# Performance work log

Measured on AMD Instinct MI355X. Metric: run time of the kernel, lower is better.

The kernel has to match this reference:

```python
import jax, jax.numpy as jnp
import numpy as np

SIGMA = (2.0, 5.0, 10.0, 20.0, 40.0, 60.0)  # RBF bandwidths from __init__
MAX_SEG = 16  # static upper bound on number of class segments (== n classes in gt)


def setup_inputs() -> dict:
    key = jax.random.key(0)
    k1, k2, k3 = jax.random.split(key, 3)
    B, C, H, W = 1, 128, 64, 64
    predict = jax.random.normal(k1, (B, C, H, W), dtype=jnp.float32)
    target = jax.random.normal(k2, (B, C, H, W), dtype=jnp.float32)
    # sorted_randint -> contiguous variable-size class segments, as the torch loop assumes
    gt = jnp.sort(jax.random.randint(k3, (B * H * W,), 0, MAX_SEG)).reshape(B, H, W)
    ignore_mask = jnp.ones((B, H, W), dtype=bool)  # all pixels visible
    return {"predict": predict, "target": target, "gt": gt, "ignore_mask": ignore_mask}


def _sqdist(a, b):
    # ||a_i - b_j||^2 ; prob_mat in the original is -0.5 * this
    aa = jnp.sum(a * a, axis=1)
    bb = jnp.sum(b * b, axis=1)
    return aa[:, None] + bb[None, :] - 2.0 * (a @ b.T)


def reference(predict, target, gt, ignore_mask):
    d = predict.shape[1]
    # [B,C,H,W] -> [V,C]; ignore_mask is all True so visible set == all pixels
    pf = predict.transpose(0, 2, 3, 1).reshape(-1, d)
    tf = target.transpose(0, 2, 3, 1).reshape(-1, d)
    cls = gt.reshape(-1)

    # segment id = index of contiguous class run (what the Python boundary loop computes)
    boundary = (cls[1:] != cls[:-1]).astype(jnp.int32)
    seg = jnp.concatenate([jnp.zeros((1,), jnp.int32), jnp.cumsum(boundary)])
    counts = jax.ops.segment_sum(jnp.ones(seg.shape, predict.dtype), seg, num_segments=MAX_SEG)

    # pairwise squared distances within/between predict and target (shared across segments)
    Dpp = _sqdist(pf, pf)
    Dtt = _sqdist(tf, tf)
    Dpt = _sqdist(pf, tf)

    # Per segment with M=N=n: ww is +1/(2n^2) on pp/tt blocks, -1/(2n^2) on cross blocks,
    # and sum over the tp block equals sum over the pt block. So
    # loss_s = (1/(2 n^2)) * sum_bw sum_{i,j in s} (Kpp + Ktt - 2 Kpt)_{ij}
    C = jnp.zeros_like(Dpp)
    for bw in SIGMA:
        inv = -0.5 / bw  # K = exp(prob/bw) = exp(-||x_i-x_j||^2 / (2 bw))
        C = C + jnp.exp(inv * Dpp) + jnp.exp(inv * Dtt) - 2.0 * jnp.exp(inv * Dpt)

    same = seg[:, None] == seg[None, :]
    C = jnp.where(same, C, 0.0)
    seg_tot = jax.ops.segment_sum(jnp.sum(C, axis=1), seg, num_segments=MAX_SEG)

    denom = jnp.maximum(2.0 * counts * counts, 1.0)
    loss_s = jnp.where(counts > 0, seg_tot / denom, 0.0)
    pos = loss_s > 0
    loss_s = jnp.where(pos, jnp.sqrt(jnp.where(pos, loss_s, 1.0)), 0.0)  # sqrt(loss) if >0 else 0

    class_count = jnp.sum(counts > 0).astype(predict.dtype)
    return jnp.sum(loss_s) / class_count
```

## Files before the change

### kernel.cpp

```cpp
#include <hip/hip_runtime.h>
#include <math.h>

#define NCLS 16
#define TILE 32
#define PAD  36
#define NB   2048
#define PIXB 16

typedef float vfloat4 __attribute__((ext_vector_type(4), aligned(4)));

struct Ctl {
    int   counts[NCLS];
    int   starts[NCLS + 1];
    int   tpc[NCLS];
    int   pairBase[NCLS + 1];
    float classSum[NCLS];
};

__global__ __launch_bounds__(256) void prep_kernel(
    const float* __restrict__ P, const float* __restrict__ T,
    const int* __restrict__ gt, int V, int D,
    Ctl* __restrict__ ctl,
    float* __restrict__ normP, float* __restrict__ normT,
    int nbNorm) {
    const int b = blockIdx.x;
    const int t = threadIdx.x;
    if (b < nbNorm) {
        __shared__ float pP[16][PIXB + 1], pT[16][PIXB + 1];
        const int pix = t & (PIXB - 1);
        const int dl  = t >> 4;
        const int v   = b * PIXB + pix;
        float np = 0.f, nt = 0.f;
        if (v < V) {
            #pragma unroll 4
            for (int d = dl; d < D; d += 16) {
                float x = P[(long)d * V + v]; np += x * x;
                float y = T[(long)d * V + v]; nt += y * y;
            }
        }
        pP[dl][pix] = np; pT[dl][pix] = nt;
        __syncthreads();
        if (t < PIXB && b * PIXB + t < V) {
            float sp = 0.f, st = 0.f;
            #pragma unroll
            for (int k = 0; k < 16; ++k) { sp += pP[k][t]; st += pT[k][t]; }
            normP[b * PIXB + t] = sp;
            normT[b * PIXB + t] = st;
        }
    } else {
        if (t < NCLS) {
            int lo = 0, hi = V;
            while (lo < hi) {
                int mid = (lo + hi) >> 1;
                if (gt[mid] < t) lo = mid + 1; else hi = mid;
            }
            ctl->starts[t] = lo;
            ctl->classSum[t] = 0.0f;
        }
        if (t == 0) ctl->starts[NCLS] = V;
        __syncthreads();
        if (t == 0) {
            int pb = 0;
            for (int c = 0; c < NCLS; ++c) {
                int n = ctl->starts[c + 1] - ctl->starts[c];
                ctl->counts[c] = n;
                int tp = (n + TILE - 1) / TILE;
                ctl->tpc[c] = tp;
                ctl->pairBase[c] = pb;
                pb += tp * tp;
            }
            ctl->pairBase[NCLS] = pb;
        }
    }
}

__global__ __launch_bounds__(256) void mmd_kernel(
    const float* __restrict__ P, const float* __restrict__ T,
    int V, int D, const Ctl* __restrict__ ctl,
    const float* __restrict__ normP, const float* __restrict__ normT,
    float* __restrict__ classSum)
{
    __shared__ float sPr[TILE][PAD], sTr[TILE][PAD];
    __shared__ float sPc[TILE][PAD], sTc[TILE][PAD];
    __shared__ float wsum[4];

    const int t  = threadIdx.x;
    const int tx = t & 15;
    const int ty = t >> 4;
    const int W  = ctl->pairBase[NCLS];

    const int sd  = (t >> 2) & 31;
    const int sr4 = ((t & 3) << 2) | ((t >> 7) << 4);

    const float invs[6] = {-0.25f, -0.1f, -0.05f, -0.025f, -0.0125f, -1.0f/120.0f};

    for (int w = blockIdx.x; w < W; w += gridDim.x) {
        int c = 0;
        while (ctl->pairBase[c + 1] <= w) ++c;
        const int local = w - ctl->pairBase[c];
        const int tp    = ctl->tpc[c];
        const int ti    = local / tp;
        const int tj    = local - ti * tp;
        const int n     = ctl->counts[c];
        const int start = ctl->starts[c];
        const int i0    = ti * TILE;
        const int j0    = tj * TILE;

        float dpp[2][2] = {{0.f,0.f},{0.f,0.f}};
        float dtt[2][2] = {{0.f,0.f},{0.f,0.f}};
        float dpt[2][2] = {{0.f,0.f},{0.f,0.f}};

        for (int dc = 0; dc < D; dc += TILE) {
            __syncthreads();
            {
                const long off   = (long)(dc + sd) * (long)V + start;
                const int  ibase = i0 + sr4;
                const int  jbase = j0 + sr4;
                vfloat4 vPr, vTr, vPc, vTc;
                if (ibase + 3 < n) {
                    vPr = *(const vfloat4*)&P[off + ibase];
                    vTr = *(const vfloat4*)&T[off + ibase];
                } else {
                    int a0 = min(ibase, n-1), a1 = min(ibase+1, n-1);
                    int a2 = min(ibase+2, n-1), a3 = min(ibase+3, n-1);
                    vPr = (vfloat4){P[off+a0], P[off+a1], P[off+a2], P[off+a3]};
                    vTr = (vfloat4){T[off+a0], T[off+a1], T[off+a2], T[off+a3]};
                }
                if (jbase + 3 < n) {
                    vPc = *(const vfloat4*)&P[off + jbase];
                    vTc = *(const vfloat4*)&T[off + jbase];
                } else {
                    int a0 = min(jbase, n-1), a1 = min(jbase+1, n-1);
                    int a2 = min(jbase+2, n-1), a3 = min(jbase+3, n-1);
                    vPc = (vfloat4){P[off+a0], P[off+a1], P[off+a2], P[off+a3]};
                    vTc = (vfloat4){T[off+a0], T[off+a1], T[off+a2], T[off+a3]};
                }
                #pragma unroll
                for (int k = 0; k < 4; ++k) {
                    sPr[sr4 + k][sd] = vPr[k];
                    sTr[sr4 + k][sd] = vTr[k];
                    sPc[sr4 + k][sd] = vPc[k];
                    sTc[sr4 + k][sd] = vTc[k];
                }
            }
            __syncthreads();

            #pragma unroll
            for (int dg = 0; dg < TILE; dg += 4) {
                float4 pr0 = *(const float4*)&sPr[ty     ][dg];
                float4 pr1 = *(const float4*)&sPr[ty + 16][dg];
                float4 tr0 = *(const float4*)&sTr[ty     ][dg];
                float4 tr1 = *(const float4*)&sTr[ty + 16][dg];
                float4 pc0 = *(const float4*)&sPc[tx     ][dg];
                float4 pc1 = *(const float4*)&sPc[tx + 16][dg];
                float4 tc0 = *(const float4*)&sTc[tx     ][dg];
                float4 tc1 = *(const float4*)&sTc[tx + 16][dg];

                dpp[0][0] += pr0.x*pc0.x + pr0.y*pc0.y + pr0.z*pc0.z + pr0.w*pc0.w;
                dpp[0][1] += pr0.x*pc1.x + pr0.y*pc1.y + pr0.z*pc1.z + pr0.w*pc1.w;
                dpp[1][0] += pr1.x*pc0.x + pr1.y*pc0.y + pr1.z*pc0.z + pr1.w*pc0.w;
                dpp[1][1] += pr1.x*pc1.x + pr1.y*pc1.y + pr1.z*pc1.z + pr1.w*pc1.w;

                dtt[0][0] += tr0.x*tc0.x + tr0.y*tc0.y + tr0.z*tc0.z + tr0.w*tc0.w;
                dtt[0][1] += tr0.x*tc1.x + tr0.y*tc1.y + tr0.z*tc1.z + tr0.w*tc1.w;
                dtt[1][0] += tr1.x*tc0.x + tr1.y*tc0.y + tr1.z*tc0.z + tr1.w*tc0.w;
                dtt[1][1] += tr1.x*tc1.x + tr1.y*tc1.y + tr1.z*tc1.z + tr1.w*tc1.w;

                dpt[0][0] += pr0.x*tc0.x + pr0.y*tc0.y + pr0.z*tc0.z + pr0.w*tc0.w;
                dpt[0][1] += pr0.x*tc1.x + pr0.y*tc1.y + pr0.z*tc1.z + pr0.w*tc1.w;
                dpt[1][0] += pr1.x*tc0.x + pr1.y*tc0.y + pr1.z*tc0.z + pr1.w*tc0.w;
                dpt[1][1] += pr1.x*tc1.x + pr1.y*tc1.y + pr1.z*tc1.z + pr1.w*tc1.w;
            }
        }

        float total = 0.0f;
        #pragma unroll
        for (int a = 0; a < 2; ++a) {
            #pragma unroll
            for (int b2 = 0; b2 < 2; ++b2) {
                int ii = i0 + ty + 16*a;
                int jj = j0 + tx + 16*b2;
                if (ii < n && jj < n) {
                    float nPi = normP[start + ii], nTi = normT[start + ii];
                    float nPj = normP[start + jj], nTj = normT[start + jj];
                    float Dpp = nPi + nPj - 2.0f * dpp[a][b2];
                    float Dtt = nTi + nTj - 2.0f * dtt[a][b2];
                    float Dpt = nPi + nTj - 2.0f * dpt[a][b2];
                    #pragma unroll
                    for (int s = 0; s < 6; ++s) {
                        total += __expf(invs[s] * Dpp)
                               + __expf(invs[s] * Dtt)
                               - 2.0f * __expf(invs[s] * Dpt);
                    }
                }
            }
        }

        #pragma unroll
        for (int off = 32; off > 0; off >>= 1)
            total += __shfl_down(total, off, 64);
        if ((t & 63) == 0) wsum[t >> 6] = total;
        __syncthreads();
        if (t == 0)
            atomicAdd(&classSum[c], wsum[0] + wsum[1] + wsum[2] + wsum[3]);
    }
}

__global__ void finalize_kernel(const int* __restrict__ counts,
                                const float* __restrict__ classSum,
                                float* __restrict__ out) {
    if (threadIdx.x == 0) {
        float loss = 0.0f;
        int k = 0;
        for (int c = 0; c < NCLS; ++c) {
            int n = counts[c];
            if (n > 0) {
                ++k;
                float fn    = (float)n;
                float denom = fmaxf(2.0f * fn * fn, 1.0f);
                float l     = classSum[c] / denom;
                if (l > 0.0f) loss += sqrtf(l);
            }
        }
        out[0] = (k > 0) ? (loss / (float)k) : 0.0f;
    }
}

extern "C" void kernel_launch(void* const* d_in, const int* in_sizes, int n_in,
                              void* d_out, int out_size, void* d_ws, size_t ws_size,
                              hipStream_t stream) {
    const float* predict = (const float*)d_in[0];
    const float* target  = (const float*)d_in[1];
    const int*   gt      = (const int*)d_in[2];

    const int V = in_sizes[2];
    const int D = in_sizes[0] / V;

    Ctl* ctl = (Ctl*)d_ws;
    size_t normOff = (sizeof(Ctl) + 15) & ~(size_t)15;
    float* normP = (float*)((char*)d_ws + normOff);
    float* normT = normP + V;
    float* classSum = (float*)((char*)d_ws + offsetof(Ctl, classSum));

    int nbNorm = (V + PIXB - 1) / PIXB;
    prep_kernel<<<nbNorm + 1, 256, 0, stream>>>(predict, target, gt, V, D,
                                                ctl, normP, normT, nbNorm);

    mmd_kernel<<<NB, 256, 0, stream>>>(predict, target, V, D, ctl,
                                       normP, normT, classSum);

    finalize_kernel<<<1, 64, 0, stream>>>(ctl->counts, classSum, (float*)d_out);
}
```

Measured before the change: 104.9 us.

## Prefetch next feature chunk into registers and vectorize norm prep kernel

```diff
diff --git a/kernel.cpp b/kernel.cpp
--- a/kernel.cpp
+++ b/kernel.cpp
@@ -5,7 +5,7 @@
 #define TILE 32
 #define PAD  36
 #define NB   2048
-#define PIXB 16
+#define PIXB 64
 
 typedef float vfloat4 __attribute__((ext_vector_type(4), aligned(4)));
 
@@ -26,26 +26,41 @@
     const int b = blockIdx.x;
     const int t = threadIdx.x;
     if (b < nbNorm) {
-        __shared__ float pP[16][PIXB + 1], pT[16][PIXB + 1];
-        const int pix = t & (PIXB - 1);
-        const int dl  = t >> 4;
-        const int v   = b * PIXB + pix;
-        float np = 0.f, nt = 0.f;
-        if (v < V) {
-            #pragma unroll 4
+        __shared__ vfloat4 sP[16][17], sT[16][17];
+        const int g    = t & 15;
+        const int dl   = t >> 4;
+        const int base = b * PIXB;
+        vfloat4 np4 = {0.f, 0.f, 0.f, 0.f};
+        vfloat4 nt4 = {0.f, 0.f, 0.f, 0.f};
+        if (base + 4 * g + 3 < V) {
             for (int d = dl; d < D; d += 16) {
-                float x = P[(long)d * V + v]; np += x * x;
-                float y = T[(long)d * V + v]; nt += y * y;
-            }
-        }
-        pP[dl][pix] = np; pT[dl][pix] = nt;
+                long idx = (long)d * V + base + 4 * g;
+                vfloat4 x = *(const vfloat4*)&P[idx];
+                vfloat4 y = *(const vfloat4*)&T[idx];
+                np4 += x * x;
+                nt4 += y * y;
+            }
+        } else {
+            for (int d = dl; d < D; d += 16) {
+                long idx = (long)d * V + base + 4 * g;
+                #pragma unroll
+                for (int k = 0; k < 4; ++k) {
+                    if (base + 4 * g + k < V) {
+                        float x = P[idx + k], y = T[idx + k];
+                        np4[k] += x * x; nt4[k] += y * y;
+                    }
+                }
+            }
+        }
+        sP[dl][g] = np4; sT[dl][g] = nt4;
         __syncthreads();
-        if (t < PIXB && b * PIXB + t < V) {
+        if (t < PIXB && base + t < V) {
+            const int gg = t >> 2, cc = t & 3;
             float sp = 0.f, st = 0.f;
             #pragma unroll
-            for (int k = 0; k < 16; ++k) { sp += pP[k][t]; st += pT[k][t]; }
-            normP[b * PIXB + t] = sp;
-            normT[b * PIXB + t] = st;
+            for (int k = 0; k < 16; ++k) { sp += sP[k][gg][cc]; st += sT[k][gg][cc]; }
+            normP[base + t] = sp;
+            normT[base + t] = st;
         }
     } else {
         if (t < NCLS) {
@@ -74,7 +89,7 @@
     }
 }
 
-__global__ __launch_bounds__(256) void mmd_kernel(
+__global__ __launch_bounds__(256, 4) void mmd_kernel(
     const float* __restrict__ P, const float* __restrict__ T,
     int V, int D, const Ctl* __restrict__ ctl,
     const float* __restrict__ normP, const float* __restrict__ normT,
@@ -106,44 +121,60 @@
         const int i0    = ti * TILE;
         const int j0    = tj * TILE;
 
+        const float nPi0 = normP[start + min(i0 + ty,      n - 1)];
+        const float nPi1 = normP[start + min(i0 + ty + 16, n - 1)];
+        const float nTi0 = normT[start + min(i0 + ty,      n - 1)];
+        const float nTi1 = normT[start + min(i0 + ty + 16, n - 1)];
+        const float nPj0 = normP[start + min(j0 + tx,      n - 1)];
+        const float nPj1 = normP[start + min(j0 + tx + 16, n - 1)];
+        const float nTj0 = normT[start + min(j0 + tx,      n - 1)];
+        const float nTj1 = normT[start + min(j0 + tx + 16, n - 1)];
+
+        const int ibase = i0 + sr4;
+        const int jbase = j0 + sr4;
+
+        auto issue_loads = [&](int dcc, vfloat4& vPr, vfloat4& vTr,
+                               vfloat4& vPc, vfloat4& vTc) {
+            const long off = (long)(dcc + sd) * (long)V + start;
+            if (ibase + 3 < n) {
+                vPr = *(const vfloat4*)&P[off + ibase];
+                vTr = *(const vfloat4*)&T[off + ibase];
+            } else {
+                int a0 = min(ibase, n-1), a1 = min(ibase+1, n-1);
+                int a2 = min(ibase+2, n-1), a3 = min(ibase+3, n-1);
+                vPr = (vfloat4){P[off+a0], P[off+a1], P[off+a2], P[off+a3]};
+                vTr = (vfloat4){T[off+a0], T[off+a1], T[off+a2], T[off+a3]};
+            }
+            if (jbase + 3 < n) {
+                vPc = *(const vfloat4*)&P[off + jbase];
+                vTc = *(const vfloat4*)&T[off + jbase];
+            } else {
+                int a0 = min(jbase, n-1), a1 = min(jbase+1, n-1);
+                int a2 = min(jbase+2, n-1), a3 = min(jbase+3, n-1);
+                vPc = (vfloat4){P[off+a0], P[off+a1], P[off+a2], P[off+a3]};
+                vTc = (vfloat4){T[off+a0], T[off+a1], T[off+a2], T[off+a3]};
+            }
+        };
+
         float dpp[2][2] = {{0.f,0.f},{0.f,0.f}};
         float dtt[2][2] = {{0.f,0.f},{0.f,0.f}};
         float dpt[2][2] = {{0.f,0.f},{0.f,0.f}};
 
+        vfloat4 vPr, vTr, vPc, vTc;
+        issue_loads(0, vPr, vTr, vPc, vTc);
+
         for (int dc = 0; dc < D; dc += TILE) {
             __syncthreads();
-            {
-                const long off   = (long)(dc + sd) * (long)V + start;
-                const int  ibase = i0 + sr4;
-                const int  jbase = j0 + sr4;
-                vfloat4 vPr, vTr, vPc, vTc;
-                if (ibase + 3 < n) {
-                    vPr = *(const vfloat4*)&P[off + ibase];
-                    vTr = *(const vfloat4*)&T[off + ibase];
-                } else {
-                    int a0 = min(ibase, n-1), a1 = min(ibase+1, n-1);
-                    int a2 = min(ibase+2, n-1), a3 = min(ibase+3, n-1);
-                    vPr = (vfloat4){P[off+a0], P[off+a1], P[off+a2], P[off+a3]};
-                    vTr = (vfloat4){T[off+a0], T[off+a1], T[off+a2], T[off+a3]};
-                }
-                if (jbase + 3 < n) {
-                    vPc = *(const vfloat4*)&P[off + jbase];
-                    vTc = *(const vfloat4*)&T[off + jbase];
-                } else {
-                    int a0 = min(jbase, n-1), a1 = min(jbase+1, n-1);
-                    int a2 = min(jbase+2, n-1), a3 = min(jbase+3, n-1);
-                    vPc = (vfloat4){P[off+a0], P[off+a1], P[off+a2], P[off+a3]};
-                    vTc = (vfloat4){T[off+a0], T[off+a1], T[off+a2], T[off+a3]};
-                }
-                #pragma unroll
-                for (int k = 0; k < 4; ++k) {
-                    sPr[sr4 + k][sd] = vPr[k];
-                    sTr[sr4 + k][sd] = vTr[k];
-                    sPc[sr4 + k][sd] = vPc[k];
-                    sTc[sr4 + k][sd] = vTc[k];
-                }
+            #pragma unroll
+            for (int k = 0; k < 4; ++k) {
+                sPr[sr4 + k][sd] = vPr[k];
+                sTr[sr4 + k][sd] = vTr[k];
+                sPc[sr4 + k][sd] = vPc[k];
+                sTc[sr4 + k][sd] = vTc[k];
             }
             __syncthreads();
+            if (dc + TILE < D)
+                issue_loads(dc + TILE, vPr, vTr, vPc, vTc);
 
             #pragma unroll
             for (int dg = 0; dg < TILE; dg += 4) {
@@ -174,6 +205,8 @@
         }
 
         float total = 0.0f;
+        const float nPi[2] = {nPi0, nPi1}, nTi[2] = {nTi0, nTi1};
+        const float nPj[2] = {nPj0, nPj1}, nTj[2] = {nTj0, nTj1};
         #pragma unroll
         for (int a = 0; a < 2; ++a) {
             #pragma unroll
@@ -181,11 +214,9 @@
                 int ii = i0 + ty + 16*a;
                 int jj = j0 + tx + 16*b2;
                 if (ii < n && jj < n) {
-                    float nPi = normP[start + ii], nTi = normT[start + ii];
-                    float nPj = normP[start + jj], nTj = normT[start + jj];
-                    float Dpp = nPi + nPj - 2.0f * dpp[a][b2];
-                    float Dtt = nTi + nTj - 2.0f * dtt[a][b2];
-                    float Dpt = nPi + nTj - 2.0f * dpt[a][b2];
+                    float Dpp = nPi[a] + nPj[b2] - 2.0f * dpp[a][b2];
+                    float Dtt = nTi[a] + nTj[b2] - 2.0f * dtt[a][b2];
+                    float Dpt = nPi[a] + nTj[b2] - 2.0f * dpt[a][b2];
                     #pragma unroll
                     for (int s = 0; s < 6; ++s) {
                         total += __expf(invs[s] * Dpp)
```

Result: slower. 202.5 us (+93.1%).

## Enlarge pair tiles to 64x64 with 4x4 register blocking and prefetch next chunk

Applied to the files above, without the earlier changes.

```diff
diff --git a/kernel.cpp b/kernel.cpp
--- a/kernel.cpp
+++ b/kernel.cpp
@@ -2,9 +2,10 @@
 #include <math.h>
 
 #define NCLS 16
-#define TILE 32
+#define TS   64
+#define CH   32
 #define PAD  36
-#define NB   2048
+#define NB   512
 #define PIXB 16
 
 typedef float vfloat4 __attribute__((ext_vector_type(4), aligned(4)));
@@ -64,7 +65,7 @@
             for (int c = 0; c < NCLS; ++c) {
                 int n = ctl->starts[c + 1] - ctl->starts[c];
                 ctl->counts[c] = n;
-                int tp = (n + TILE - 1) / TILE;
+                int tp = (n + TS - 1) / TS;
                 ctl->tpc[c] = tp;
                 ctl->pairBase[c] = pb;
                 pb += tp * tp;
@@ -80,17 +81,16 @@
     const float* __restrict__ normP, const float* __restrict__ normT,
     float* __restrict__ classSum)
 {
-    __shared__ float sPr[TILE][PAD], sTr[TILE][PAD];
-    __shared__ float sPc[TILE][PAD], sTc[TILE][PAD];
+    __shared__ float sPr[TS][PAD], sTr[TS][PAD];
+    __shared__ float sPc[TS][PAD], sTc[TS][PAD];
     __shared__ float wsum[4];
 
     const int t  = threadIdx.x;
     const int tx = t & 15;
     const int ty = t >> 4;
+    const int sd = t >> 3;
+    const int qb = t & 7;
     const int W  = ctl->pairBase[NCLS];
-
-    const int sd  = (t >> 2) & 31;
-    const int sr4 = ((t & 3) << 2) | ((t >> 7) << 4);
 
     const float invs[6] = {-0.25f, -0.1f, -0.05f, -0.025f, -0.0125f, -1.0f/120.0f};
 
@@ -103,94 +103,109 @@
         const int tj    = local - ti * tp;
         const int n     = ctl->counts[c];
         const int start = ctl->starts[c];
-        const int i0    = ti * TILE;
-        const int j0    = tj * TILE;
-
-        float dpp[2][2] = {{0.f,0.f},{0.f,0.f}};
-        float dtt[2][2] = {{0.f,0.f},{0.f,0.f}};
-        float dpt[2][2] = {{0.f,0.f},{0.f,0.f}};
-
-        for (int dc = 0; dc < D; dc += TILE) {
+        const int i0    = ti * TS;
+        const int j0    = tj * TS;
+
+        const int r0 = i0 + 4 * qb;
+        const int r1 = i0 + 4 * qb + 32;
+        const int c0 = j0 + 4 * qb;
+        const int c1 = j0 + 4 * qb + 32;
+
+        vfloat4 vPr0, vPr1, vTr0, vTr1, vPc0, vPc1, vTc0, vTc1;
+
+        auto load_quad = [&](long off, int rb, vfloat4& vP, vfloat4& vT) {
+            if (rb + 3 < n) {
+                vP = *(const vfloat4*)&P[off + start + rb];
+                vT = *(const vfloat4*)&T[off + start + rb];
+            } else {
+                int a0 = start + min(rb,     n - 1);
+                int a1 = start + min(rb + 1, n - 1);
+                int a2 = start + min(rb + 2, n - 1);
+                int a3 = start + min(rb + 3, n - 1);
+                vP = (vfloat4){P[off + a0], P[off + a1], P[off + a2], P[off + a3]};
+                vT = (vfloat4){T[off + a0], T[off + a1], T[off + a2], T[off + a3]};
+            }
+        };
+        auto issue_loads = [&](int dcc) {
+            const long off = (long)(dcc + sd) * (long)V;
+            load_quad(off, r0, vPr0, vTr0);
+            load_quad(off, r1, vPr1, vTr1);
+            load_quad(off, c0, vPc0, vTc0);
+            load_quad(off, c1, vPc1, vTc1);
+        };
+
+        float dpp[4][4], dtt[4][4], dpt[4][4];
+        #pragma unroll
+        for (int a = 0; a < 4; ++a)
+            #pragma unroll
+            for (int b = 0; b < 4; ++b) { dpp[a][b] = 0.f; dtt[a][b] = 0.f; dpt[a][b] = 0.f; }
+
+        issue_loads(0);
+
+        for (int dc = 0; dc < D; dc += CH) {
             __syncthreads();
-            {
-                const long off   = (long)(dc + sd) * (long)V + start;
-                const int  ibase = i0 + sr4;
-                const int  jbase = j0 + sr4;
-                vfloat4 vPr, vTr, vPc, vTc;
-                if (ibase + 3 < n) {
-                    vPr = *(const vfloat4*)&P[off + ibase];
-                    vTr = *(const vfloat4*)&T[off + ibase];
-                } else {
-                    int a0 = min(ibase, n-1), a1 = min(ibase+1, n-1);
-                    int a2 = min(ibase+2, n-1), a3 = min(ibase+3, n-1);
-                    vPr = (vfloat4){P[off+a0], P[off+a1], P[off+a2], P[off+a3]};
-                    vTr = (vfloat4){T[off+a0], T[off+a1], T[off+a2], T[off+a3]};
-                }
-                if (jbase + 3 < n) {
-                    vPc = *(const vfloat4*)&P[off + jbase];
-                    vTc = *(const vfloat4*)&T[off + jbase];
-                } else {
-                    int a0 = min(jbase, n-1), a1 = min(jbase+1, n-1);
-                    int a2 = min(jbase+2, n-1), a3 = min(jbase+3, n-1);
-                    vPc = (vfloat4){P[off+a0], P[off+a1], P[off+a2], P[off+a3]};
-                    vTc = (vfloat4){T[off+a0], T[off+a1], T[off+a2], T[off+a3]};
+            #pragma unroll
+            for (int k = 0; k < 4; ++k) {
+                sPr[4*qb +      k][sd] = vPr0[k];
+                sPr[4*qb + 32 + k][sd] = vPr1[k];
+                sTr[4*qb +      k][sd] = vTr0[k];
+                sTr[4*qb + 32 + k][sd] = vTr1[k];
+                sPc[4*qb +      k][sd] = vPc0[k];
+                sPc[4*qb + 32 + k][sd] = vPc1[k];
+                sTc[4*qb +      k][sd] = vTc0[k];
+                sTc[4*qb + 32 + k][sd] = vTc1[k];
+            }
+            __syncthreads();
+            if (dc + CH < D)
+                issue_loads(dc + CH);
+
+            #pragma unroll
+            for (int dg = 0; dg < CH; dg += 4) {
+                float4 rP[4], rT[4], cP[4], cT[4];
+                #pragma unroll
+                for (int a = 0; a < 4; ++a) {
+                    rP[a] = *(const float4*)&sPr[ty + 16*a][dg];
+                    rT[a] = *(const float4*)&sTr[ty + 16*a][dg];
+                    cP[a] = *(const float4*)&sPc[tx + 16*a][dg];
+                    cT[a] = *(const float4*)&sTc[tx + 16*a][dg];
                 }
                 #pragma unroll
-                for (int k = 0; k < 4; ++k) {
-                    sPr[sr4 + k][sd] = vPr[k];
-                    sTr[sr4 + k][sd] = vTr[k];
-                    sPc[sr4 + k][sd] = vPc[k];
-                    sTc[sr4 + k][sd] = vTc[k];
+                for (int a = 0; a < 4; ++a) {
+                    #pragma unroll
+                    for (int b = 0; b < 4; ++b) {
+                        dpp[a][b] += rP[a].x*cP[b].x + rP[a].y*cP[b].y
+                                   + rP[a].z*cP[b].z + rP[a].w*cP[b].w;
+                        dtt[a][b] += rT[a].x*cT[b].x + rT[a].y*cT[b].y
+                                   + rT[a].z*cT[b].z + rT[a].w*cT[b].w;
+                        dpt[a][b] += rP[a].x*cT[b].x + rP[a].y*cT[b].y
+                                   + rP[a].z*cT[b].z + rP[a].w*cT[b].w;
+                    }
                 }
-            }
-            __syncthreads();
-
-            #pragma unroll
-            for (int dg = 0; dg < TILE; dg += 4) {
-                float4 pr0 = *(const float4*)&sPr[ty     ][dg];
-                float4 pr1 = *(const float4*)&sPr[ty + 16][dg];
-                float4 tr0 = *(const float4*)&sTr[ty     ][dg];
-                float4 tr1 = *(const float4*)&sTr[ty + 16][dg];
-                float4 pc0 = *(const float4*)&sPc[tx     ][dg];
-                float4 pc1 = *(const float4*)&sPc[tx + 16][dg];
-                float4 tc0 = *(const float4*)&sTc[tx     ][dg];
-                float4 tc1 = *(const float4*)&sTc[tx + 16][dg];
-
-                dpp[0][0] += pr0.x*pc0.x + pr0.y*pc0.y + pr0.z*pc0.z + pr0.w*pc0.w;
-                dpp[0][1] += pr0.x*pc1.x + pr0.y*pc1.y + pr0.z*pc1.z + pr0.w*pc1.w;
-                dpp[1][0] += pr1.x*pc0.x + pr1.y*pc0.y + pr1.z*pc0.z + pr1.w*pc0.w;
-                dpp[1][1] += pr1.x*pc1.x + pr1.y*pc1.y + pr1.z*pc1.z + pr1.w*pc1.w;
-
-                dtt[0][0] += tr0.x*tc0.x + tr0.y*tc0.y + tr0.z*tc0.z + tr0.w*tc0.w;
-                dtt[0][1] += tr0.x*tc1.x + tr0.y*tc1.y + tr0.z*tc1.z + tr0.w*tc1.w;
-                dtt[1][0] += tr1.x*tc0.x + tr1.y*tc0.y + tr1.z*tc0.z + tr1.w*tc0.w;
-                dtt[1][1] += tr1.x*tc1.x + tr1.y*tc1.y + tr1.z*tc1.z + tr1.w*tc1.w;
-
-                dpt[0][0] += pr0.x*tc0.x + pr0.y*tc0.y + pr0.z*tc0.z + pr0.w*tc0.w;
-                dpt[0][1] += pr0.x*tc1.x + pr0.y*tc1.y + pr0.z*tc1.z + pr0.w*tc1.w;
-                dpt[1][0] += pr1.x*tc0.x + pr1.y*tc0.y + pr1.z*tc0.z + pr1.w*tc0.w;
-                dpt[1][1] += pr1.x*tc1.x + pr1.y*tc1.y + pr1.z*tc1.z + pr1.w*tc1.w;
             }
         }
 
         float total = 0.0f;
         #pragma unroll
-        for (int a = 0; a < 2; ++a) {
-            #pragma unroll
-            for (int b2 = 0; b2 < 2; ++b2) {
-                int ii = i0 + ty + 16*a;
-                int jj = j0 + tx + 16*b2;
-                if (ii < n && jj < n) {
-                    float nPi = normP[start + ii], nTi = normT[start + ii];
-                    float nPj = normP[start + jj], nTj = normT[start + jj];
-                    float Dpp = nPi + nPj - 2.0f * dpp[a][b2];
-                    float Dtt = nTi + nTj - 2.0f * dtt[a][b2];
-                    float Dpt = nPi + nTj - 2.0f * dpt[a][b2];
-                    #pragma unroll
-                    for (int s = 0; s < 6; ++s) {
-                        total += __expf(invs[s] * Dpp)
-                               + __expf(invs[s] * Dtt)
-                               - 2.0f * __expf(invs[s] * Dpt);
+        for (int a = 0; a < 4; ++a) {
+            const int ii = i0 + ty + 16*a;
+            if (ii < n) {
+                const float nPi = normP[start + ii];
+                const float nTi = normT[start + ii];
+                #pragma unroll
+                for (int b = 0; b < 4; ++b) {
+                    const int jj = j0 + tx + 16*b;
+                    if (jj < n) {
+                        const float nPj = normP[start + jj];
+                        const float nTj = normT[start + jj];
+                        float Dpp = nPi + nPj - 2.0f * dpp[a][b];
+                        float Dtt = nTi + nTj - 2.0f * dtt[a][b];
+                        float Dpt = nPi + nTj - 2.0f * dpt[a][b];
+                        #pragma unroll
+                        for (int s = 0; s < 6; ++s) {
+                            total += __expf(invs[s] * Dpp)
+                                   + __expf(invs[s] * Dtt)
+                                   - 2.0f * __expf(invs[s] * Dpt);
+                        }
                     }
                 }
             }
```

Result: slower. 170.0 us (+62.1%).
